# Performance work log

Hardware: AMD Instinct MI355X
Metric: run time of the kernel (lower is better)

## Reference

```python
import jax, jax.numpy as jnp
import numpy as np


def _params_to_tokens(params):
    # (batch, 2k) -> (batch, k, 2) : chunk into freqs/amps then stack
    freqs, amps = jnp.split(params, 2, axis=-1)
    return jnp.stack((freqs, amps), axis=-1)


def setup_inputs() -> dict:
    key = jax.random.key(0)
    k1, k2 = jax.random.split(key)
    predicted = jax.random.normal(k1, (64, 4096), dtype=jnp.float32)
    target = jax.random.normal(k2, (64, 4096), dtype=jnp.float32)
    return {"predicted": predicted, "target": target}


def reference(predicted, target):
    p = _params_to_tokens(predicted)   # (b, k, 2)
    t = _params_to_tokens(target)      # (b, k, 2)
    # Euclidean cdist via gram-matrix identity (avoids (b,k,k,2) broadcast temp)
    p2 = jnp.sum(p * p, axis=-1)       # (b, k)
    t2 = jnp.sum(t * t, axis=-1)       # (b, k)
    gram = jnp.einsum('bid,bjd->bij', p, t)  # (b, k, k)
    sq = p2[:, :, None] + t2[:, None, :] - 2.0 * gram
    costs = jnp.sqrt(jnp.maximum(sq, 0.0))   # (b, k, k)
    min1 = jnp.mean(jnp.min(costs, axis=1), axis=-1)  # min over predicted dim
    min2 = jnp.mean(jnp.min(costs, axis=2), axis=-1)  # min over target dim
    return jnp.mean(min1 + min2)
```

## Files before the change

kernel.cpp:

```cpp
#include <hip/hip_runtime.h>


typedef _Float16 f16;
typedef _Float16 f16x8 __attribute__((ext_vector_type(8)));
typedef float f32x16 __attribute__((ext_vector_type(16)));

constexpr int K = 2048;
constexpr int BLOCK = 512;
constexpr int NBAND = 8;
constexpr int BAND = 256;
constexpr int NJT = K / 32;
constexpr unsigned INF_U = 0x7F800000u;

#define MFMA16 __builtin_amdgcn_mfma_f32_32x32x16_f16

__device__ __forceinline__ unsigned pk(f16 lo, f16 hi) {
  unsigned a = (unsigned)__builtin_bit_cast(unsigned short, lo);
  unsigned b = (unsigned)__builtin_bit_cast(unsigned short, hi);
  return a | (b << 16);
}
__device__ __forceinline__ unsigned split2(float v) {
  const f16 h = (f16)v;
  const f16 l = (f16)(v - (float)h);
  return pk(h, l);
}
__device__ __forceinline__ float min3p(float a, float b, float c) {
  return fminf(fminf(a, b), c);
}

__global__ __launch_bounds__(BLOCK, 4) void chamfer_mfma(
    const float* __restrict__ pred, const float* __restrict__ targ,
    float* __restrict__ out, float* __restrict__ ws) {
  const int iband = blockIdx.x;
  const int b = blockIdx.y;
  const int tid = threadIdx.x;
  const int lane = tid & 63;
  const int w = tid >> 6;
  const int r = lane & 31;
  const bool lo_half = (lane < 32);

  __shared__ uint4 BrecP[K + 1];
  __shared__ uint4 ArecP[2 * BAND];
  __shared__ unsigned colmin_u[K];
  __shared__ float wsum[8];

  const float* tb = targ + (size_t)b * (2 * K);
  const float* pb = pred + (size_t)b * (2 * K);

  #pragma unroll
  for (int k = 0; k < K / BLOCK; ++k) {
    const int j = tid + k * BLOCK;
    const float x = tb[j], y = tb[K + j];
    const unsigned wx = split2(x);
    const unsigned wy = split2(y);
    const unsigned wt = split2(fmaf(x, x, y * y));
    BrecP[j] = make_uint4(wx,
                          (wx & 0xffffu) | (wy << 16),
                          (wy >> 16) | (wy << 16),
                          wt);
    colmin_u[j] = INF_U;
  }
  if (tid == 0) BrecP[K] = make_uint4(0x3C003C00u, 0u, 0u, 0u);
  if (tid < BAND) {
    const int i = iband * BAND + tid;
    const float x = pb[i], y = pb[K + i];
    const unsigned wu = split2(-2.0f * x);
    const unsigned ww = split2(-2.0f * y);
    const unsigned wp = split2(fmaf(x, x, y * y));
    ArecP[tid] = make_uint4((wu & 0xffffu) | (wu << 16),
                            (wu >> 16) | (ww << 16),
                            ww,
                            0x3C003C00u);
    ArecP[BAND + tid] = make_uint4(wp, 0u, 0u, 0u);
  }
  __syncthreads();

  const f32x16 zero = {};

  const f16x8 af = __builtin_bit_cast(
      f16x8, ArecP[(lo_half ? 0 : BAND) + w * 32 + r]);

  f32x16 rowacc;
  #pragma unroll
  for (int q = 0; q < 16; ++q) rowacc[q] = 3.4e38f;

  int bidx = lo_half ? r : (int)K;
  const int bstep = lo_half ? 32 : 0;

  for (int jt = 0; jt < NJT; jt += 4) {
    const uint4 q0 = BrecP[bidx];
    const uint4 q1 = BrecP[bidx + bstep];
    const uint4 q2 = BrecP[bidx + 2 * bstep];
    const uint4 q3 = BrecP[bidx + 3 * bstep];
    bidx += 4 * bstep;

    const f32x16 d0 = MFMA16(af, __builtin_bit_cast(f16x8, q0), zero, 0, 0, 0);
    const f32x16 d1 = MFMA16(af, __builtin_bit_cast(f16x8, q1), zero, 0, 0, 0);
    const f32x16 d2 = MFMA16(af, __builtin_bit_cast(f16x8, q2), zero, 0, 0, 0);
    const f32x16 d3 = MFMA16(af, __builtin_bit_cast(f16x8, q3), zero, 0, 0, 0);

    #pragma unroll
    for (int q = 0; q < 16; ++q)
      rowacc[q] = min3p(rowacc[q], d0[q], d1[q]);
    #pragma unroll
    for (int q = 0; q < 16; ++q)
      rowacc[q] = min3p(rowacc[q], d2[q], d3[q]);

    {
      const float t0 = min3p(d0[0], d0[1], d0[2]);
      const float t1 = min3p(d0[3], d0[4], d0[5]);
      const float t2 = min3p(d0[6], d0[7], d0[8]);
      const float t3 = min3p(d0[9], d0[10], d0[11]);
      const float t4 = min3p(d0[12], d0[13], d0[14]);
      float cm = fminf(min3p(t0, t1, t2), min3p(t3, t4, d0[15]));
      cm = fmaxf(cm, 0.0f);
      atomicMin(&colmin_u[(jt + 0) * 32 + r], __float_as_uint(cm));
    }
    {
      const float t0 = min3p(d1[0], d1[1], d1[2]);
      const float t1 = min3p(d1[3], d1[4], d1[5]);
      const float t2 = min3p(d1[6], d1[7], d1[8]);
      const float t3 = min3p(d1[9], d1[10], d1[11]);
      const float t4 = min3p(d1[12], d1[13], d1[14]);
      float cm = fminf(min3p(t0, t1, t2), min3p(t3, t4, d1[15]));
      cm = fmaxf(cm, 0.0f);
      atomicMin(&colmin_u[(jt + 1) * 32 + r], __float_as_uint(cm));
    }
    {
      const float t0 = min3p(d2[0], d2[1], d2[2]);
      const float t1 = min3p(d2[3], d2[4], d2[5]);
      const float t2 = min3p(d2[6], d2[7], d2[8]);
      const float t3 = min3p(d2[9], d2[10], d2[11]);
      const float t4 = min3p(d2[12], d2[13], d2[14]);
      float cm = fminf(min3p(t0, t1, t2), min3p(t3, t4, d2[15]));
      cm = fmaxf(cm, 0.0f);
      atomicMin(&colmin_u[(jt + 2) * 32 + r], __float_as_uint(cm));
    }
    {
      const float t0 = min3p(d3[0], d3[1], d3[2]);
      const float t1 = min3p(d3[3], d3[4], d3[5]);
      const float t2 = min3p(d3[6], d3[7], d3[8]);
      const float t3 = min3p(d3[9], d3[10], d3[11]);
      const float t4 = min3p(d3[12], d3[13], d3[14]);
      float cm = fminf(min3p(t0, t1, t2), min3p(t3, t4, d3[15]));
      cm = fmaxf(cm, 0.0f);
      atomicMin(&colmin_u[(jt + 3) * 32 + r], __float_as_uint(cm));
    }
  }

  #pragma unroll
  for (int m = 1; m <= 16; m <<= 1) {
    #pragma unroll
    for (int q = 0; q < 16; ++q)
      rowacc[q] = fminf(rowacc[q], __shfl_xor(rowacc[q], m, 64));
  }
  float s = 0.0f;
  #pragma unroll
  for (int q = 0; q < 16; ++q) s += sqrtf(fmaxf(rowacc[q], 0.0f));
  s += __shfl_xor(s, 32, 64);
  if (lane == 0) wsum[w] = s;
  __syncthreads();
  if (tid == 0) {
    float t = 0.0f;
    #pragma unroll
    for (int i = 0; i < 8; ++i) t += wsum[i];
    atomicAdd(out, t * (1.0f / 131072.0f));
  }
  float* wrow = ws + (size_t)(b * NBAND + iband) * K;
  #pragma unroll
  for (int k = 0; k < K / BLOCK; ++k) {
    const int j = tid + k * BLOCK;
    wrow[j] = __uint_as_float(colmin_u[j]);
  }
}

__global__ __launch_bounds__(256, 4) void chamfer_pass2(
    const float* __restrict__ ws, float* __restrict__ out) {
  const int b = blockIdx.x;
  const int tid = threadIdx.x;
  __shared__ float wsum[4];
  const float* wrow = ws + (size_t)b * NBAND * K;
  float s = 0.0f;
  #pragma unroll
  for (int k = 0; k < K / 256; ++k) {
    const int j = tid + k * 256;
    float m = wrow[j];
    #pragma unroll
    for (int band = 1; band < NBAND; ++band) m = fminf(m, wrow[band * K + j]);
    s += sqrtf(m);
  }
  #pragma unroll
  for (int off = 32; off; off >>= 1) s += __shfl_down(s, off, 64);
  const int lane = tid & 63, w = tid >> 6;
  if (lane == 0) wsum[w] = s;
  __syncthreads();
  if (tid == 0)
    atomicAdd(out, (wsum[0] + wsum[1] + wsum[2] + wsum[3]) * (1.0f / 131072.0f));
}

extern "C" void kernel_launch(void* const* d_in, const int* in_sizes, int n_in,
                              void* d_out, int out_size, void* d_ws, size_t ws_size,
                              hipStream_t stream) {
  const float* pred = (const float*)d_in[0];
  const float* targ = (const float*)d_in[1];
  float* out = (float*)d_out;
  float* ws = (float*)d_ws;

  dim3 g1(NBAND, 64);
  chamfer_mfma<<<g1, dim3(BLOCK), 0, stream>>>(pred, targ, out, ws);
  chamfer_pass2<<<dim3(64), dim3(256), 0, stream>>>(ws, out);
}
```

Baseline: 80.10 us.

## Software-pipeline B-record loads with 2-tile steps and raise occupancy to 6 blocks

The main loop now processes two 32-column tiles per iteration instead of four and prefetches the next pair of LDS records while the current MFMAs and min-reductions run, with the last pair peeled into an epilogue. Launch bounds change from 4 to 6 blocks per CU, which caps register use so more waves can be resident. The aim is to hide LDS latency and raise occupancy; the cost is less ILP per wave, more loop overhead, and possible register spills under the tighter cap.

After: 80.16 us. No clear change (+0.1%).

```diff
diff --git a/kernel.cpp b/kernel.cpp
--- a/kernel.cpp
+++ b/kernel.cpp
@@ -28,7 +28,18 @@
   return fminf(fminf(a, b), c);
 }
 
-__global__ __launch_bounds__(BLOCK, 4) void chamfer_mfma(
+__device__ __forceinline__ void colfold(const f32x16& d, unsigned* addr) {
+  const float t0 = min3p(d[0], d[1], d[2]);
+  const float t1 = min3p(d[3], d[4], d[5]);
+  const float t2 = min3p(d[6], d[7], d[8]);
+  const float t3 = min3p(d[9], d[10], d[11]);
+  const float t4 = min3p(d[12], d[13], d[14]);
+  float cm = fminf(min3p(t0, t1, t2), min3p(t3, t4, d[15]));
+  cm = fmaxf(cm, 0.0f);
+  atomicMin(addr, __float_as_uint(cm));
+}
+
+__global__ __launch_bounds__(BLOCK, 6) void chamfer_mfma(
     const float* __restrict__ pred, const float* __restrict__ targ,
     float* __restrict__ out, float* __restrict__ ws) {
   const int iband = blockIdx.x;
@@ -87,65 +98,38 @@
   int bidx = lo_half ? r : (int)K;
   const int bstep = lo_half ? 32 : 0;
 
-  for (int jt = 0; jt < NJT; jt += 4) {
-    const uint4 q0 = BrecP[bidx];
-    const uint4 q1 = BrecP[bidx + bstep];
-    const uint4 q2 = BrecP[bidx + 2 * bstep];
-    const uint4 q3 = BrecP[bidx + 3 * bstep];
-    bidx += 4 * bstep;
+  uint4 c0 = BrecP[bidx];
+  uint4 c1 = BrecP[bidx + bstep];
+  bidx += 2 * bstep;
 
-    const f32x16 d0 = MFMA16(af, __builtin_bit_cast(f16x8, q0), zero, 0, 0, 0);
-    const f32x16 d1 = MFMA16(af, __builtin_bit_cast(f16x8, q1), zero, 0, 0, 0);
-    const f32x16 d2 = MFMA16(af, __builtin_bit_cast(f16x8, q2), zero, 0, 0, 0);
-    const f32x16 d3 = MFMA16(af, __builtin_bit_cast(f16x8, q3), zero, 0, 0, 0);
+  #pragma unroll 1
+  for (int jt = 0; jt < NJT - 2; jt += 2) {
+    const uint4 n0 = BrecP[bidx];
+    const uint4 n1 = BrecP[bidx + bstep];
+    bidx += 2 * bstep;
+
+    const f32x16 d0 = MFMA16(af, __builtin_bit_cast(f16x8, c0), zero, 0, 0, 0);
+    const f32x16 d1 = MFMA16(af, __builtin_bit_cast(f16x8, c1), zero, 0, 0, 0);
 
     #pragma unroll
     for (int q = 0; q < 16; ++q)
       rowacc[q] = min3p(rowacc[q], d0[q], d1[q]);
+
+    colfold(d0, &colmin_u[jt * 32 + r]);
+    colfold(d1, &colmin_u[jt * 32 + 32 + r]);
+
+    c0 = n0;
+    c1 = n1;
+  }
+  {
+    const int jt = NJT - 2;
+    const f32x16 d0 = MFMA16(af, __builtin_bit_cast(f16x8, c0), zero, 0, 0, 0);
+    const f32x16 d1 = MFMA16(af, __builtin_bit_cast(f16x8, c1), zero, 0, 0, 0);
     #pragma unroll
     for (int q = 0; q < 16; ++q)
-      rowacc[q] = min3p(rowacc[q], d2[q], d3[q]);
-
-    {
-      const float t0 = min3p(d0[0], d0[1], d0[2]);
-      const float t1 = min3p(d0[3], d0[4], d0[5]);
-      const float t2 = min3p(d0[6], d0[7], d0[8]);
-      const float t3 = min3p(d0[9], d0[10], d0[11]);
-      const float t4 = min3p(d0[12], d0[13], d0[14]);
-      float cm = fminf(min3p(t0, t1, t2), min3p(t3, t4, d0[15]));
-      cm = fmaxf(cm, 0.0f);
-      atomicMin(&colmin_u[(jt + 0) * 32 + r], __float_as_uint(cm));
-    }
-    {
-      const float t0 = min3p(d1[0], d1[1], d1[2]);
-      const float t1 = min3p(d1[3], d1[4], d1[5]);
-      const float t2 = min3p(d1[6], d1[7], d1[8]);
-      const float t3 = min3p(d1[9], d1[10], d1[11]);
-      const float t4 = min3p(d1[12], d1[13], d1[14]);
-      float cm = fminf(min3p(t0, t1, t2), min3p(t3, t4, d1[15]));
-      cm = fmaxf(cm, 0.0f);
-      atomicMin(&colmin_u[(jt + 1) * 32 + r], __float_as_uint(cm));
-    }
-    {
-      const float t0 = min3p(d2[0], d2[1], d2[2]);
-      const float t1 = min3p(d2[3], d2[4], d2[5]);
-      const float t2 = min3p(d2[6], d2[7], d2[8]);
-      const float t3 = min3p(d2[9], d2[10], d2[11]);
-      const float t4 = min3p(d2[12], d2[13], d2[14]);
-      float cm = fminf(min3p(t0, t1, t2), min3p(t3, t4, d2[15]));
-      cm = fmaxf(cm, 0.0f);
-      atomicMin(&colmin_u[(jt + 2) * 32 + r], __float_as_uint(cm));
-    }
-    {
-      const float t0 = min3p(d3[0], d3[1], d3[2]);
-      const float t1 = min3p(d3[3], d3[4], d3[5]);
-      const float t2 = min3p(d3[6], d3[7], d3[8]);
-      const float t3 = min3p(d3[9], d3[10], d3[11]);
-      const float t4 = min3p(d3[12], d3[13], d3[14]);
-      float cm = fminf(min3p(t0, t1, t2), min3p(t3, t4, d3[15]));
-      cm = fmaxf(cm, 0.0f);
-      atomicMin(&colmin_u[(jt + 3) * 32 + r], __float_as_uint(cm));
-    }
+      rowacc[q] = min3p(rowacc[q], d0[q], d1[q]);
+    colfold(d0, &colmin_u[jt * 32 + r]);
+    colfold(d1, &colmin_u[jt * 32 + 32 + r]);
   }
 
   #pragma unroll
```
